# Kernel tuning notes

Hardware: AMD Instinct MI355X
Metric: run time of the kernel (lower is better)

## Reference

```python
import jax, jax.numpy as jnp
import numpy as np

EPS = 1e-5

def setup_inputs() -> dict:
    key = jax.random.key(0)
    k1, k2, k3 = jax.random.split(key, 3)
    x = jax.random.normal(k1, (16, 256, 32, 32), dtype=jnp.float32)
    embed = jax.random.normal(k2, (8192, 256), dtype=jnp.float32)
    cluster_size = jax.random.uniform(k3, (8192,), dtype=jnp.float32)
    return {"x": x, "embed": embed, "cluster_size": cluster_size}

def reference(x, embed, cluster_size):
    # x: (b, c, h, w) -> (b, h*w, c); project_in is Identity (codebook_dim == dim, heads=1)
    b, c, h, w = x.shape
    xt = jnp.transpose(x, (0, 2, 3, 1)).reshape(b, h * w, c)   # (b, n, d)
    flat = xt.reshape(-1, c)                                    # (N, d)
    d2 = (jnp.sum(flat * flat, axis=1, keepdims=True)
          - 2.0 * flat @ embed.T
          + jnp.sum(embed * embed, axis=1))                     # (N, K)
    embed_ind_flat = jnp.argmin(d2, axis=-1)                    # (N,) temperature==0 -> argmax of -d2
    quantize = embed[embed_ind_flat].reshape(b, h * w, c)       # gather codebook rows
    embed_ind = embed_ind_flat.reshape(b, h * w)
    # perplexity over (unnormalized) EMA cluster sizes, as in the torch code
    probs = cluster_size
    perplexity = jnp.exp(-jnp.sum(probs * jnp.log(probs + EPS)))
    # eval-mode commitment loss (weight_loss=True, commitment_weight=1.0)
    commit_loss = jnp.mean((quantize - xt) ** 2)
    return quantize, embed_ind, perplexity, commit_loss
```

## Files before the change

kernel.cpp:

```cpp
#include <hip/hip_runtime.h>
#include <hip/hip_bf16.h>
#include <math.h>

typedef _Float16 f16x8 __attribute__((ext_vector_type(8)));
typedef float f32x4 __attribute__((ext_vector_type(4)));

#define N_TOK 16384
#define D 256
#define K 8192

#define Q_OFF 0
#define IND_OFF 4194304
#define PERP_OFF 4210688
#define COMMIT_OFF 4210689

#define WS_CAND   0u
#define WS_E2     1048576u
#define WS_DSUM   1081344u
#define WS_EH     1114112u
#define WS_XH     5308416u
#define WS_XT     13697024u
#define WS_NEED   30474240u

__device__ __forceinline__ unsigned int ford(float f) {
    unsigned int u = __float_as_uint(f);
    return (u & 0x80000000u) ? ~u : (u | 0x80000000u);
}
__device__ __forceinline__ unsigned short f2h(float f) {
    _Float16 h = (_Float16)f;
    return *(unsigned short*)&h;
}
__device__ __forceinline__ void gload16(const void* g, void* l) {
    __builtin_amdgcn_global_load_lds(
        (const __attribute__((address_space(1))) unsigned int*)g,
        (__attribute__((address_space(3))) unsigned int*)l, 16, 0, 0);
}


__global__ void vq_convert_x(const float* __restrict__ x, float* __restrict__ xt,
                             unsigned short* __restrict__ xh) {
    __shared__ float t[64][65];
    const int tid = threadIdx.x;
    const int p0 = blockIdx.x * 64, c0 = blockIdx.y * 64, b = blockIdx.z;
    const int q = tid & 15, h = tid >> 4;
    #pragma unroll
    for (int r = 0; r < 4; ++r) {
        const int cl = r * 16 + h;
        const float4 v = *(const float4*)(x + (((size_t)(b * 256 + c0 + cl)) << 10) + p0 + q * 4);
        t[cl][q * 4 + 0] = v.x; t[cl][q * 4 + 1] = v.y;
        t[cl][q * 4 + 2] = v.z; t[cl][q * 4 + 3] = v.w;
    }
    __syncthreads();
    #pragma unroll
    for (int r = 0; r < 4; ++r) {
        const int nl = r * 16 + h;
        const int n = (b << 10) + p0 + nl;
        const int c = c0 + q * 4;
        float4 vf; ushort4 vh;
        vf.x = t[q * 4 + 0][nl]; vf.y = t[q * 4 + 1][nl];
        vf.z = t[q * 4 + 2][nl]; vf.w = t[q * 4 + 3][nl];
        vh.x = f2h(vf.x); vh.y = f2h(vf.y); vh.z = f2h(vf.z); vh.w = f2h(vf.w);
        *(float4*)(xt + ((size_t)n << 8) + c) = vf;
        *(ushort4*)(xh + ((size_t)n << 8) + c) = vh;
    }
}

__global__ void vq_prep_e(const float* __restrict__ e, unsigned short* __restrict__ eh,
                          float* __restrict__ e2, double* __restrict__ dsum) {
    if (blockIdx.x == 0 && threadIdx.x == 0) *dsum = 0.0;
    const int wave = threadIdx.x >> 6, lane = threadIdx.x & 63;
    const int c = blockIdx.x * 4 + wave;
    const float4 v = *(const float4*)(e + (size_t)c * D + lane * 4);
    ushort4 vh;
    vh.x = f2h(v.x); vh.y = f2h(v.y); vh.z = f2h(v.z); vh.w = f2h(v.w);
    *(ushort4*)(eh + (size_t)c * D + lane * 4) = vh;
    float s = v.x * v.x + v.y * v.y + v.z * v.z + v.w * v.w;
    #pragma unroll
    for (int off = 32; off > 0; off >>= 1) s += __shfl_down(s, off, 64);
    if (lane == 0) e2[c] = s;
}

__global__ __launch_bounds__(256)
__attribute__((amdgpu_waves_per_eu(2, 2)))
void vq_mfma_kernel(
    const unsigned short* __restrict__ xh, const unsigned short* __restrict__ eh,
    const float* __restrict__ e2, unsigned int* __restrict__ cand) {
    __shared__ __align__(16) unsigned short Bs[3][32 * 256];
    __shared__ float e2s[1024];

    const int tid = threadIdx.x;
    const int lane = tid & 63, wid = tid >> 6;
    const int l15 = lane & 15, lg = lane >> 4;
    const int split = blockIdx.y;
    const int m0 = blockIdx.x * 256;
    const int c0s = split * 1024;
    const int rw = m0 + wid * 64;

    *(float4*)&e2s[tid * 4] = *(const float4*)(e2 + c0s + tid * 4);

    f16x8 a[4][8];
    #pragma unroll
    for (int mf = 0; mf < 4; ++mf) {
        const unsigned short* ap = xh + (((size_t)(rw + mf * 16 + l15)) << 8) + lg * 8;
        #pragma unroll
        for (int t = 0; t < 8; ++t)
            a[mf][t] = *(const f16x8*)(ap + t * 32);
    }
    #pragma unroll
    for (int mf = 0; mf < 4; ++mf)
        #pragma unroll
        for (int t = 0; t < 8; ++t)
            asm volatile("" : "+v"(*(f32x4*)&a[mf][t]));

    __syncthreads();

    const int r0 = tid >> 5, cc = tid & 31;
    const unsigned short* ebase =
        eh + (((size_t)(c0s + r0)) << 8) + ((cc ^ (r0 & 7)) << 3);
    char* wdst = (char*)Bs + tid * 16;

    auto stage = [&](int t, int bo) {
        const unsigned short* p = ebase + t * 8192;
        #pragma unroll
        for (int i = 0; i < 4; ++i)
            gload16(p + i * 2048, wdst + bo + i * 4096);
    };

    const int rb0 = l15 * 512;
    const int rb1 = rb0 + 16 * 512;
    const int rx = l15 & 7;
    const char* wb = (const char*)Bs;

    float d1[16], d2[16];
    unsigned int ipk[16];
    #pragma unroll
    for (int r = 0; r < 16; ++r) { d1[r] = INFINITY; d2[r] = INFINITY; ipk[r] = 0; }

    int bo0 = 0, bo1 = 16384, bo2 = 32768;
    stage(0, bo0);
    stage(1, bo1);

    #pragma unroll 1
    for (int t = 0; t < 32; ++t) {
        if (t < 31) asm volatile("s_waitcnt vmcnt(4)" ::: "memory");
        else        asm volatile("s_waitcnt vmcnt(0)" ::: "memory");
        __builtin_amdgcn_s_barrier();
        if (t < 30) stage(t + 2, bo2);

        const float e2v0 = e2s[t * 32 + l15];
        const float e2v1 = e2s[t * 32 + 16 + l15];
        f32x4 acc[4][2];
        #pragma unroll
        for (int mf = 0; mf < 4; ++mf) {
            f32x4 z = {0.f, 0.f, 0.f, 0.f};
            acc[mf][0] = z; acc[mf][1] = z;
        }
        __builtin_amdgcn_s_setprio(1);
        #pragma unroll
        for (int ks = 0; ks < 4; ++ks) {
            #pragma unroll
            for (int ks2 = 0; ks2 < 2; ++ks2) {
                const int kc = ks * 8 + ks2 * 4;
                const int ko = ((kc + lg) ^ rx) << 4;
                const f16x8 b0 = *(const f16x8*)(wb + bo0 + rb0 + ko);
                const f16x8 b1 = *(const f16x8*)(wb + bo0 + rb1 + ko);
                #pragma unroll
                for (int mf = 0; mf < 4; ++mf) {
                    acc[mf][0] = __builtin_amdgcn_mfma_f32_16x16x32_f16(
                        a[mf][ks * 2 + ks2], b0, acc[mf][0], 0, 0, 0);
                    acc[mf][1] = __builtin_amdgcn_mfma_f32_16x16x32_f16(
                        a[mf][ks * 2 + ks2], b1, acc[mf][1], 0, 0, 0);
                }
            }
        }
        __builtin_amdgcn_s_setprio(0);

        const unsigned int cl0 = (unsigned int)(t * 32 + l15);
        #pragma unroll
        for (int mf = 0; mf < 4; ++mf) {
            #pragma unroll
            for (int reg = 0; reg < 4; ++reg) {
                const int rr = mf * 4 + reg;
                const float sc0 = fmaf(-2.0f, acc[mf][0][reg], e2v0);
                const float sc1 = fmaf(-2.0f, acc[mf][1][reg], e2v1);
                if (fminf(sc0, sc1) < d2[rr]) {
                    {
                        const bool lt1 = sc0 < d1[rr], lt2 = sc0 < d2[rr];
                        const unsigned int ii = ipk[rr];
                        const unsigned int nif = (ii << 16) | cl0;
                        const unsigned int nis = (ii & 0xFFFFu) | (cl0 << 16);
                        d2[rr] = lt1 ? d1[rr] : (lt2 ? sc0 : d2[rr]);
                        ipk[rr] = lt1 ? nif : (lt2 ? nis : ii);
                        d1[rr] = lt1 ? sc0 : d1[rr];
                    }
                    {
                        const unsigned int cl1 = cl0 + 16;
                        const bool lt1 = sc1 < d1[rr], lt2 = sc1 < d2[rr];
                        const unsigned int ii = ipk[rr];
                        const unsigned int nif = (ii << 16) | cl1;
                        const unsigned int nis = (ii & 0xFFFFu) | (cl1 << 16);
                        d2[rr] = lt1 ? d1[rr] : (lt2 ? sc1 : d2[rr]);
                        ipk[rr] = lt1 ? nif : (lt2 ? nis : ii);
                        d1[rr] = lt1 ? sc1 : d1[rr];
                    }
                }
            }
        }
        const int tmp = bo0; bo0 = bo1; bo1 = bo2; bo2 = tmp;
    }

    unsigned long long p1[16], p2[16];
    #pragma unroll
    for (int r = 0; r < 16; ++r) {
        p1[r] = (((unsigned long long)ford(d1[r])) << 32) |
                (unsigned int)(c0s + (ipk[r] & 0xFFFFu));
        p2[r] = (((unsigned long long)ford(d2[r])) << 32) |
                (unsigned int)(c0s + (ipk[r] >> 16));
    }
    #pragma unroll
    for (int st = 1; st < 16; st <<= 1) {
        #pragma unroll
        for (int r = 0; r < 16; ++r) {
            const unsigned long long q1 = __shfl_xor(p1[r], st, 64);
            const unsigned long long q2 = __shfl_xor(p2[r], st, 64);
            const unsigned long long n1 = p1[r] < q1 ? p1[r] : q1;
            const unsigned long long hi = p1[r] < q1 ? q1 : p1[r];
            const unsigned long long l2 = p2[r] < q2 ? p2[r] : q2;
            p1[r] = n1;
            p2[r] = hi < l2 ? hi : l2;
        }
    }
    if (l15 == 0) {
        #pragma unroll
        for (int mf = 0; mf < 4; ++mf)
            #pragma unroll
            for (int reg = 0; reg < 4; ++reg) {
                const int n = rw + mf * 16 + lg * 4 + reg;
                unsigned int* cp = cand + (((size_t)n) << 4) + split * 2;
                cp[0] = (unsigned int)p1[mf * 4 + reg];
                cp[1] = (unsigned int)p2[mf * 4 + reg];
            }
    }
}

__global__ void vq_rescore_finalize(const float* __restrict__ xt, const float* __restrict__ embed,
                                    const float* __restrict__ e2,
                                    const unsigned int* __restrict__ cand,
                                    float* __restrict__ out, double* __restrict__ dsum) {
    __shared__ double red[4];
    const int tid = threadIdx.x, wid = tid >> 6, lane = tid & 63;
    double wsum = 0.0;
    #pragma unroll 1
    for (int it = 0; it < 8; ++it) {
        const int n = blockIdx.x * 32 + it * 4 + wid;
        const float4 xv = *(const float4*)(xt + (((size_t)n) << 8) + lane * 4);
        unsigned long long best = 0xFFFFFFFFFFFFFFFFull;
        #pragma unroll 2
        for (int j = 0; j < 16; ++j) {
            const unsigned int c = cand[(((size_t)n) << 4) + j];
            const float4 ev = *(const float4*)(embed + (((size_t)c) << 8) + lane * 4);
            float dt = xv.x * ev.x + xv.y * ev.y + xv.z * ev.z + xv.w * ev.w;
            #pragma unroll
            for (int off = 32; off > 0; off >>= 1) dt += __shfl_xor(dt, off, 64);
            const float s = fmaf(-2.0f, dt, e2[c]);
            const unsigned long long p = (((unsigned long long)ford(s)) << 32) | c;
            best = p < best ? p : best;
        }
        const unsigned int bi = (unsigned int)(best & 0xFFFFFFFFull);
        if (lane == 0) out[IND_OFF + n] = (float)bi;
        const float4 ev = *(const float4*)(embed + (((size_t)bi) << 8) + lane * 4);
        *(float4*)(out + Q_OFF + (((size_t)n) << 8) + lane * 4) = ev;
        const float q0 = ev.x - xv.x, q1 = ev.y - xv.y, q2 = ev.z - xv.z, q3 = ev.w - xv.w;
        float a4 = q0 * q0 + q1 * q1 + q2 * q2 + q3 * q3;
        #pragma unroll
        for (int off = 32; off > 0; off >>= 1) a4 += __shfl_xor(a4, off, 64);
        if (lane == 0) wsum += (double)a4;
    }
    if (lane == 0) red[wid] = wsum;
    __syncthreads();
    if (tid == 0) atomicAdd(dsum, red[0] + red[1] + red[2] + red[3]);
}

__global__ void vq_tail_kernel(const float* __restrict__ cs,
                               const double* __restrict__ dsum,
                               float* __restrict__ out) {
    __shared__ double red[4];
    const int tid = threadIdx.x;
    double s = 0.0;
    for (int i = tid; i < K; i += 256) {
        const float p = cs[i];
        s += (double)(p * logf(p + 1e-5f));
    }
    #pragma unroll
    for (int off = 32; off > 0; off >>= 1) s += __shfl_down(s, off, 64);
    if ((tid & 63) == 0) red[tid >> 6] = s;
    __syncthreads();
    if (tid == 0) {
        const double tot = red[0] + red[1] + red[2] + red[3];
        const double pv = exp(-tot);
        out[PERP_OFF] = (pv > 3.3e38) ? 3.3e38f : (float)pv;
        out[COMMIT_OFF] = (float)(*dsum * (1.0 / 4194304.0));
    }
}

#define TM 64
#define TN 64
#define BKF 32
#define NSPLITF 2
#define CODES_PER_SPLIT (K / NSPLITF)
#define TILES_PER_SPLIT (CODES_PER_SPLIT / TN)

__global__ void vq_init_kernel(unsigned long long* __restrict__ keys, double* __restrict__ dsum) {
    int i = blockIdx.x * blockDim.x + threadIdx.x;
    if (i < N_TOK) keys[i] = 0xFFFFFFFFFFFFFFFFull;
    if (i == 0) *dsum = 0.0;
}
__global__ void vq_e2_kernel(const float* __restrict__ embed, float* __restrict__ e2) {
    int wave = threadIdx.x >> 6, lane = threadIdx.x & 63;
    int c = blockIdx.x * 4 + wave;
    const float4 v = *(const float4*)(embed + (size_t)c * D + lane * 4);
    float s = v.x * v.x + v.y * v.y + v.z * v.z + v.w * v.w;
    #pragma unroll
    for (int off = 32; off > 0; off >>= 1) s += __shfl_down(s, off, 64);
    if (lane == 0) e2[c] = s;
}
__global__ __launch_bounds__(256, 2) void vq_argmin_kernel(
    const float* __restrict__ x, const float* __restrict__ embed,
    const float* __restrict__ e2, unsigned long long* __restrict__ keys) {
    __shared__ float xT[D][TM];
    __shared__ float eT[BKF][TN + 4];
    const int tid = threadIdx.x;
    const int n0 = blockIdx.x * TM;
    const int b = n0 >> 10, p0 = n0 & 1023;
    const float* xb = x + (size_t)b * D * 1024 + p0;
    {
        const int t4 = (tid & 15) * 4, chb = tid >> 4;
        #pragma unroll
        for (int pass = 0; pass < 16; ++pass) {
            const int ch = pass * 16 + chb;
            *(float4*)&xT[ch][t4] = *(const float4*)(xb + (size_t)ch * 1024 + t4);
        }
    }
    __syncthreads();
    const int tm4 = (tid & 15) * 4, tn = tid >> 4, tn4 = tn * 4;
    float bestd[4]; int besti[4];
    #pragma unroll
    for (int i = 0; i < 4; ++i) { bestd[i] = INFINITY; besti[i] = 0x7fffffff; }
    for (int ct = 0; ct < TILES_PER_SPLIT; ++ct) {
        const int c0 = blockIdx.y * CODES_PER_SPLIT + ct * TN;
        float acc[4][4] = {};
        for (int kk = 0; kk < D; kk += BKF) {
            {
                const int j = tid >> 2, ch4 = (tid & 3) * 4;
                #pragma unroll
                for (int p = 0; p < 2; ++p) {
                    const int chl = p * 16 + ch4;
                    const float4 ev = *(const float4*)(embed + (size_t)(c0 + j) * D + kk + chl);
                    eT[chl + 0][j] = ev.x; eT[chl + 1][j] = ev.y;
                    eT[chl + 2][j] = ev.z; eT[chl + 3][j] = ev.w;
                }
            }
            __syncthreads();
            #pragma unroll
            for (int k2 = 0; k2 < BKF; ++k2) {
                const float4 a = *(const float4*)&xT[kk + k2][tm4];
                const float4 bv = *(const float4*)&eT[k2][tn4];
                acc[0][0] += a.x * bv.x; acc[0][1] += a.x * bv.y; acc[0][2] += a.x * bv.z; acc[0][3] += a.x * bv.w;
                acc[1][0] += a.y * bv.x; acc[1][1] += a.y * bv.y; acc[1][2] += a.y * bv.z; acc[1][3] += a.y * bv.w;
                acc[2][0] += a.z * bv.x; acc[2][1] += a.z * bv.y; acc[2][2] += a.z * bv.z; acc[2][3] += a.z * bv.w;
                acc[3][0] += a.w * bv.x; acc[3][1] += a.w * bv.y; acc[3][2] += a.w * bv.z; acc[3][3] += a.w * bv.w;
            }
            __syncthreads();
        }
        #pragma unroll
        for (int j = 0; j < 4; ++j) {
            const int c = c0 + tn4 + j;
            const float ec = e2[c];
            #pragma unroll
            for (int i = 0; i < 4; ++i) {
                const float s = ec - 2.0f * acc[i][j];
                if (s < bestd[i]) { bestd[i] = s; besti[i] = c; }
            }
        }
    }
    __syncthreads();
    float* cd = &eT[0][0];
    int* ci = (int*)&eT[16][0];
    #pragma unroll
    for (int i = 0; i < 4; ++i) { cd[tn * 64 + tm4 + i] = bestd[i]; ci[tn * 64 + tm4 + i] = besti[i]; }
    __syncthreads();
    if (tid < TM) {
        float bd = INFINITY; int bi = 0x7fffffff;
        for (int j = 0; j < 16; ++j) {
            const float d = cd[j * 64 + tid]; const int idx = ci[j * 64 + tid];
            if (d < bd || (d == bd && idx < bi)) { bd = d; bi = idx; }
        }
        atomicMin(&keys[n0 + tid], (((unsigned long long)ford(bd)) << 32) | (unsigned int)bi);
    }
}
__global__ void vq_finalize_kernel(const float* __restrict__ x, const float* __restrict__ embed,
                                   const unsigned long long* __restrict__ keys,
                                   float* __restrict__ out, double* __restrict__ dsum) {
    const int tid = threadIdx.x;
    const int n0 = blockIdx.x * 64;
    const int t = tid >> 2, q = tid & 3;
    const int n = n0 + t;
    const int b = n >> 10, p = n & 1023;
    if (tid < 64) {
        const int nn = n0 + tid;
        out[IND_OFF + nn] = (float)(int)(unsigned int)(keys[nn] & 0xFFFFFFFFull);
    }
    const int idx = (int)(unsigned int)(keys[n] & 0xFFFFFFFFull);
    const float* erow = embed + (size_t)idx * D;
    const float* xrow = x + (size_t)b * D * 1024 + p;
    float* qrow = out + Q_OFF + (size_t)n * D;
    float acc = 0.0f;
    #pragma unroll
    for (int i = 0; i < 16; ++i) {
        const int ch = i * 16 + q * 4;
        const float4 ev = *(const float4*)(erow + ch);
        *(float4*)(qrow + ch) = ev;
        const float x0 = xrow[(size_t)(ch + 0) * 1024];
        const float x1 = xrow[(size_t)(ch + 1) * 1024];
        const float x2 = xrow[(size_t)(ch + 2) * 1024];
        const float x3 = xrow[(size_t)(ch + 3) * 1024];
        const float d0 = ev.x - x0, d1 = ev.y - x1, d2 = ev.z - x2, d3 = ev.w - x3;
        acc += d0 * d0 + d1 * d1 + d2 * d2 + d3 * d3;
    }
    #pragma unroll
    for (int off = 32; off > 0; off >>= 1) acc += __shfl_down(acc, off, 64);
    if ((tid & 63) == 0) atomicAdd(dsum, (double)acc);
}

extern "C" void kernel_launch(void* const* d_in, const int* in_sizes, int n_in,
                              void* d_out, int out_size, void* d_ws, size_t ws_size,
                              hipStream_t stream) {
    const float* x = (const float*)d_in[0];
    const float* embed = (const float*)d_in[1];
    const float* cs = (const float*)d_in[2];
    float* out = (float*)d_out;
    char* ws = (char*)d_ws;

    if (ws_size >= (size_t)WS_NEED) {
        unsigned int* cand = (unsigned int*)(ws + WS_CAND);
        float* e2 = (float*)(ws + WS_E2);
        double* dsum = (double*)(ws + WS_DSUM);
        unsigned short* eh = (unsigned short*)(ws + WS_EH);
        unsigned short* xh = (unsigned short*)(ws + WS_XH);
        float* xt = (float*)(ws + WS_XT);

        vq_prep_e<<<dim3(K / 4), dim3(256), 0, stream>>>(embed, eh, e2, dsum);
        vq_convert_x<<<dim3(16, 4, 16), dim3(256), 0, stream>>>(x, xt, xh);
        vq_mfma_kernel<<<dim3(64, 8), dim3(256), 0, stream>>>(xh, eh, e2, cand);
        vq_rescore_finalize<<<dim3(512), dim3(256), 0, stream>>>(xt, embed, e2, cand, out, dsum);
        vq_tail_kernel<<<dim3(1), dim3(256), 0, stream>>>(cs, dsum, out);
    } else {
        unsigned long long* keys = (unsigned long long*)ws;
        float* e2 = (float*)(ws + 131072);
        double* dsum = (double*)(ws + 163840);
        vq_init_kernel<<<dim3(64), dim3(256), 0, stream>>>(keys, dsum);
        vq_e2_kernel<<<dim3(K / 4), dim3(256), 0, stream>>>(embed, e2);
        vq_argmin_kernel<<<dim3(N_TOK / TM, NSPLITF), dim3(256), 0, stream>>>(x, embed, e2, keys);
        vq_finalize_kernel<<<dim3(256), dim3(256), 0, stream>>>(x, embed, keys, out, dsum);
        vq_tail_kernel<<<dim3(1), dim3(256), 0, stream>>>(cs, dsum, out);
    }
}
```

Measured before the change: 173.2 us.

## Switch to double-buffered 64-row codebook tiles with software-prefetched LDS fragments

Replaces the triple-buffered 32-row codebook staging with two 64-row buffers, so each barrier covers twice as much work and there are half as many iterations. Within a tile, the B fragments for the next k-step are loaded from LDS before the current MFMAs issue, a register-level software pipeline. The change also drops the setprio hints and waits for all outstanding loads (vmcnt(0)) before every barrier. That wait removes the two-ahead prefetch depth, which risks exposing global load latency. The XOR swizzle now uses the full row index.

New measurement: 167.6 us. 3.3% less time.

```diff
diff --git a/kernel.cpp b/kernel.cpp
--- a/kernel.cpp
+++ b/kernel.cpp
@@ -85,7 +85,7 @@
 void vq_mfma_kernel(
     const unsigned short* __restrict__ xh, const unsigned short* __restrict__ eh,
     const float* __restrict__ e2, unsigned int* __restrict__ cand) {
-    __shared__ __align__(16) unsigned short Bs[3][32 * 256];
+    __shared__ __align__(16) unsigned short Bs[2][64 * 256];
     __shared__ float e2s[1024];
 
     const int tid = threadIdx.x;
@@ -116,97 +116,95 @@
 
     const int r0 = tid >> 5, cc = tid & 31;
     const unsigned short* ebase =
-        eh + (((size_t)(c0s + r0)) << 8) + ((cc ^ (r0 & 7)) << 3);
+        eh + (((size_t)(c0s + r0)) << 8) + ((cc ^ r0) << 3);
     char* wdst = (char*)Bs + tid * 16;
-
     auto stage = [&](int t, int bo) {
-        const unsigned short* p = ebase + t * 8192;
-        #pragma unroll
-        for (int i = 0; i < 4; ++i)
+        const unsigned short* p = ebase + t * 16384;
+        #pragma unroll
+        for (int i = 0; i < 8; ++i)
             gload16(p + i * 2048, wdst + bo + i * 4096);
     };
 
-    const int rb0 = l15 * 512;
-    const int rb1 = rb0 + 16 * 512;
-    const int rx = l15 & 7;
-    const char* wb = (const char*)Bs;
+    const char* rbase = (const char*)Bs + l15 * 512;
+    int ko[8];
+    #pragma unroll
+    for (int pr = 0; pr < 8; ++pr) ko[pr] = (((4 * pr + lg) ^ (l15 & 7)) << 4);
 
     float d1[16], d2[16];
     unsigned int ipk[16];
     #pragma unroll
     for (int r = 0; r < 16; ++r) { d1[r] = INFINITY; d2[r] = INFINITY; ipk[r] = 0; }
 
-    int bo0 = 0, bo1 = 16384, bo2 = 32768;
-    stage(0, bo0);
-    stage(1, bo1);
-
-    #pragma unroll 1
-    for (int t = 0; t < 32; ++t) {
-        if (t < 31) asm volatile("s_waitcnt vmcnt(4)" ::: "memory");
-        else        asm volatile("s_waitcnt vmcnt(0)" ::: "memory");
+    stage(0, 0);
+
+    #pragma unroll 2
+    for (int t = 0; t < 16; ++t) {
+        asm volatile("s_waitcnt vmcnt(0)" ::: "memory");
         __builtin_amdgcn_s_barrier();
-        if (t < 30) stage(t + 2, bo2);
-
-        const float e2v0 = e2s[t * 32 + l15];
-        const float e2v1 = e2s[t * 32 + 16 + l15];
-        f32x4 acc[4][2];
-        #pragma unroll
-        for (int mf = 0; mf < 4; ++mf) {
-            f32x4 z = {0.f, 0.f, 0.f, 0.f};
-            acc[mf][0] = z; acc[mf][1] = z;
-        }
-        __builtin_amdgcn_s_setprio(1);
-        #pragma unroll
-        for (int ks = 0; ks < 4; ++ks) {
-            #pragma unroll
-            for (int ks2 = 0; ks2 < 2; ++ks2) {
-                const int kc = ks * 8 + ks2 * 4;
-                const int ko = ((kc + lg) ^ rx) << 4;
-                const f16x8 b0 = *(const f16x8*)(wb + bo0 + rb0 + ko);
-                const f16x8 b1 = *(const f16x8*)(wb + bo0 + rb1 + ko);
+        if (t < 15) stage(t + 1, ((t + 1) & 1) * 32768);
+
+        const int BUF = (t & 1) * 32768;
+        #pragma unroll
+        for (int s2 = 0; s2 < 2; ++s2) {
+            const int sb = BUF + s2 * 16384;
+            const float e2v0 = e2s[t * 64 + s2 * 32 + l15];
+            const float e2v1 = e2s[t * 64 + s2 * 32 + 16 + l15];
+            f32x4 acc[4][2];
+            #pragma unroll
+            for (int mf = 0; mf < 4; ++mf) {
+                f32x4 z = {0.f, 0.f, 0.f, 0.f};
+                acc[mf][0] = z; acc[mf][1] = z;
+            }
+            f16x8 b0a = *(const f16x8*)(rbase + ko[0] + sb);
+            f16x8 b1a = *(const f16x8*)(rbase + ko[0] + sb + 8192);
+            #pragma unroll
+            for (int pr = 0; pr < 8; ++pr) {
+                f16x8 b0n, b1n;
+                if (pr < 7) {
+                    b0n = *(const f16x8*)(rbase + ko[pr + 1] + sb);
+                    b1n = *(const f16x8*)(rbase + ko[pr + 1] + sb + 8192);
+                }
                 #pragma unroll
                 for (int mf = 0; mf < 4; ++mf) {
                     acc[mf][0] = __builtin_amdgcn_mfma_f32_16x16x32_f16(
-                        a[mf][ks * 2 + ks2], b0, acc[mf][0], 0, 0, 0);
+                        a[mf][pr], b0a, acc[mf][0], 0, 0, 0);
                     acc[mf][1] = __builtin_amdgcn_mfma_f32_16x16x32_f16(
-                        a[mf][ks * 2 + ks2], b1, acc[mf][1], 0, 0, 0);
+                        a[mf][pr], b1a, acc[mf][1], 0, 0, 0);
                 }
-            }
-        }
-        __builtin_amdgcn_s_setprio(0);
-
-        const unsigned int cl0 = (unsigned int)(t * 32 + l15);
-        #pragma unroll
-        for (int mf = 0; mf < 4; ++mf) {
-            #pragma unroll
-            for (int reg = 0; reg < 4; ++reg) {
-                const int rr = mf * 4 + reg;
-                const float sc0 = fmaf(-2.0f, acc[mf][0][reg], e2v0);
-                const float sc1 = fmaf(-2.0f, acc[mf][1][reg], e2v1);
-                if (fminf(sc0, sc1) < d2[rr]) {
-                    {
-                        const bool lt1 = sc0 < d1[rr], lt2 = sc0 < d2[rr];
-                        const unsigned int ii = ipk[rr];
-                        const unsigned int nif = (ii << 16) | cl0;
-                        const unsigned int nis = (ii & 0xFFFFu) | (cl0 << 16);
-                        d2[rr] = lt1 ? d1[rr] : (lt2 ? sc0 : d2[rr]);
-                        ipk[rr] = lt1 ? nif : (lt2 ? nis : ii);
-                        d1[rr] = lt1 ? sc0 : d1[rr];
-                    }
-                    {
-                        const unsigned int cl1 = cl0 + 16;
-                        const bool lt1 = sc1 < d1[rr], lt2 = sc1 < d2[rr];
-                        const unsigned int ii = ipk[rr];
-                        const unsigned int nif = (ii << 16) | cl1;
-                        const unsigned int nis = (ii & 0xFFFFu) | (cl1 << 16);
-                        d2[rr] = lt1 ? d1[rr] : (lt2 ? sc1 : d2[rr]);
-                        ipk[rr] = lt1 ? nif : (lt2 ? nis : ii);
-                        d1[rr] = lt1 ? sc1 : d1[rr];
+                b0a = b0n; b1a = b1n;
+            }
+            const unsigned int cl0 = (unsigned int)(t * 64 + s2 * 32 + l15);
+            #pragma unroll
+            for (int mf = 0; mf < 4; ++mf) {
+                #pragma unroll
+                for (int reg = 0; reg < 4; ++reg) {
+                    const int rr = mf * 4 + reg;
+                    const float sc0 = fmaf(-2.0f, acc[mf][0][reg], e2v0);
+                    const float sc1 = fmaf(-2.0f, acc[mf][1][reg], e2v1);
+                    if (fminf(sc0, sc1) < d2[rr]) {
+                        {
+                            const bool lt1 = sc0 < d1[rr], lt2 = sc0 < d2[rr];
+                            const unsigned int ii = ipk[rr];
+                            const unsigned int nif = (ii << 16) | cl0;
+                            const unsigned int nis = (ii & 0xFFFFu) | (cl0 << 16);
+                            d2[rr] = lt1 ? d1[rr] : (lt2 ? sc0 : d2[rr]);
+                            ipk[rr] = lt1 ? nif : (lt2 ? nis : ii);
+                            d1[rr] = lt1 ? sc0 : d1[rr];
+                        }
+                        {
+                            const unsigned int cl1 = cl0 + 16;
+                            const bool lt1 = sc1 < d1[rr], lt2 = sc1 < d2[rr];
+                            const unsigned int ii = ipk[rr];
+                            const unsigned int nif = (ii << 16) | cl1;
+                            const unsigned int nis = (ii & 0xFFFFu) | (cl1 << 16);
+                            d2[rr] = lt1 ? d1[rr] : (lt2 ? sc1 : d2[rr]);
+                            ipk[rr] = lt1 ? nif : (lt2 ? nis : ii);
+                            d1[rr] = lt1 ? sc1 : d1[rr];
+                        }
                     }
                 }
             }
         }
-        const int tmp = bo0; bo0 = bo1; bo1 = bo2; bo2 = tmp;
     }
 
     unsigned long long p1[16], p2[16];
```

## Pre-swizzle codebook into MFMA fragment layout and load B directly from global

Applied to the files above, without the earlier changes.

The fp16 codebook is now written in a tiled layout that matches the MFMA B-operand fragment, so each lane can load its fragments with contiguous 16-byte global loads. The LDS triple-buffered async staging, barriers and waves-per-eu hint are removed, and the loop works on 16-column tiles instead of 32. This drops LDS traffic and per-tile block synchronisation, but B loads are no longer shared across the four waves (each wave fetches the same data, relying on L1/L2) and there is no explicit prefetch, so memory latency may be exposed.

Result: slower. 196.4 us (+13.4%).

```diff
diff --git a/kernel.cpp b/kernel.cpp
--- a/kernel.cpp
+++ b/kernel.cpp
@@ -29,11 +29,6 @@
 __device__ __forceinline__ unsigned short f2h(float f) {
     _Float16 h = (_Float16)f;
     return *(unsigned short*)&h;
-}
-__device__ __forceinline__ void gload16(const void* g, void* l) {
-    __builtin_amdgcn_global_load_lds(
-        (const __attribute__((address_space(1))) unsigned int*)g,
-        (__attribute__((address_space(3))) unsigned int*)l, 16, 0, 0);
 }
 
 
@@ -65,7 +60,7 @@
     }
 }
 
-__global__ void vq_prep_e(const float* __restrict__ e, unsigned short* __restrict__ eh,
+__global__ void vq_prep_e(const float* __restrict__ e, unsigned short* __restrict__ ehT,
                           float* __restrict__ e2, double* __restrict__ dsum) {
     if (blockIdx.x == 0 && threadIdx.x == 0) *dsum = 0.0;
     const int wave = threadIdx.x >> 6, lane = threadIdx.x & 63;
@@ -73,7 +68,9 @@
     const float4 v = *(const float4*)(e + (size_t)c * D + lane * 4);
     ushort4 vh;
     vh.x = f2h(v.x); vh.y = f2h(v.y); vh.z = f2h(v.z); vh.w = f2h(v.w);
-    *(ushort4*)(eh + (size_t)c * D + lane * 4) = vh;
+    unsigned short* dst = ehT + (((size_t)(c >> 4)) << 12) + ((lane >> 1) << 7) +
+                          ((c & 15) << 3) + ((lane & 1) << 2);
+    *(ushort4*)dst = vh;
     float s = v.x * v.x + v.y * v.y + v.z * v.z + v.w * v.w;
     #pragma unroll
     for (int off = 32; off > 0; off >>= 1) s += __shfl_down(s, off, 64);
@@ -81,11 +78,9 @@
 }
 
 __global__ __launch_bounds__(256)
-__attribute__((amdgpu_waves_per_eu(2, 2)))
 void vq_mfma_kernel(
-    const unsigned short* __restrict__ xh, const unsigned short* __restrict__ eh,
+    const unsigned short* __restrict__ xh, const unsigned short* __restrict__ ehT,
     const float* __restrict__ e2, unsigned int* __restrict__ cand) {
-    __shared__ __align__(16) unsigned short Bs[3][32 * 256];
     __shared__ float e2s[1024];
 
     const int tid = threadIdx.x;
@@ -106,107 +101,49 @@
         for (int t = 0; t < 8; ++t)
             a[mf][t] = *(const f16x8*)(ap + t * 32);
     }
-    #pragma unroll
-    for (int mf = 0; mf < 4; ++mf)
-        #pragma unroll
-        for (int t = 0; t < 8; ++t)
-            asm volatile("" : "+v"(*(f32x4*)&a[mf][t]));
-
-    __syncthreads();
-
-    const int r0 = tid >> 5, cc = tid & 31;
-    const unsigned short* ebase =
-        eh + (((size_t)(c0s + r0)) << 8) + ((cc ^ (r0 & 7)) << 3);
-    char* wdst = (char*)Bs + tid * 16;
-
-    auto stage = [&](int t, int bo) {
-        const unsigned short* p = ebase + t * 8192;
-        #pragma unroll
-        for (int i = 0; i < 4; ++i)
-            gload16(p + i * 2048, wdst + bo + i * 4096);
-    };
-
-    const int rb0 = l15 * 512;
-    const int rb1 = rb0 + 16 * 512;
-    const int rx = l15 & 7;
-    const char* wb = (const char*)Bs;
+    __syncthreads();
+
+    const char* bb = (const char*)ehT + (((size_t)c0s) << 9) + lane * 16;
 
     float d1[16], d2[16];
     unsigned int ipk[16];
     #pragma unroll
     for (int r = 0; r < 16; ++r) { d1[r] = INFINITY; d2[r] = INFINITY; ipk[r] = 0; }
 
-    int bo0 = 0, bo1 = 16384, bo2 = 32768;
-    stage(0, bo0);
-    stage(1, bo1);
-
     #pragma unroll 1
-    for (int t = 0; t < 32; ++t) {
-        if (t < 31) asm volatile("s_waitcnt vmcnt(4)" ::: "memory");
-        else        asm volatile("s_waitcnt vmcnt(0)" ::: "memory");
-        __builtin_amdgcn_s_barrier();
-        if (t < 30) stage(t + 2, bo2);
-
-        const float e2v0 = e2s[t * 32 + l15];
-        const float e2v1 = e2s[t * 32 + 16 + l15];
-        f32x4 acc[4][2];
+    for (int tile = 0; tile < 64; ++tile) {
+        const char* tb = bb + tile * 8192;
+        f16x8 b[8];
+        #pragma unroll
+        for (int j = 0; j < 8; ++j) b[j] = *(const f16x8*)(tb + j * 1024);
+        const float e2v = e2s[tile * 16 + l15];
+        f32x4 acc[4];
         #pragma unroll
         for (int mf = 0; mf < 4; ++mf) {
             f32x4 z = {0.f, 0.f, 0.f, 0.f};
-            acc[mf][0] = z; acc[mf][1] = z;
-        }
-        __builtin_amdgcn_s_setprio(1);
-        #pragma unroll
-        for (int ks = 0; ks < 4; ++ks) {
-            #pragma unroll
-            for (int ks2 = 0; ks2 < 2; ++ks2) {
-                const int kc = ks * 8 + ks2 * 4;
-                const int ko = ((kc + lg) ^ rx) << 4;
-                const f16x8 b0 = *(const f16x8*)(wb + bo0 + rb0 + ko);
-                const f16x8 b1 = *(const f16x8*)(wb + bo0 + rb1 + ko);
-                #pragma unroll
-                for (int mf = 0; mf < 4; ++mf) {
-                    acc[mf][0] = __builtin_amdgcn_mfma_f32_16x16x32_f16(
-                        a[mf][ks * 2 + ks2], b0, acc[mf][0], 0, 0, 0);
-                    acc[mf][1] = __builtin_amdgcn_mfma_f32_16x16x32_f16(
-                        a[mf][ks * 2 + ks2], b1, acc[mf][1], 0, 0, 0);
+            acc[mf] = z;
+        }
+        #pragma unroll
+        for (int j = 0; j < 8; ++j)
+            #pragma unroll
+            for (int mf = 0; mf < 4; ++mf)
+                acc[mf] = __builtin_amdgcn_mfma_f32_16x16x32_f16(
+                    a[mf][j], b[j], acc[mf], 0, 0, 0);
+        const unsigned int cl = (unsigned int)(tile * 16 + l15);
+        #pragma unroll
+        for (int mf = 0; mf < 4; ++mf)
+            #pragma unroll
+            for (int reg = 0; reg < 4; ++reg) {
+                const int rr = mf * 4 + reg;
+                const float s = fmaf(-2.0f, acc[mf][reg], e2v);
+                if (s < d2[rr]) {
+                    const bool lt1 = s < d1[rr];
+                    const unsigned int ii = ipk[rr];
+                    d2[rr] = lt1 ? d1[rr] : s;
+                    ipk[rr] = lt1 ? ((ii << 16) | cl) : ((ii & 0xFFFFu) | (cl << 16));
+                    d1[rr] = lt1 ? s : d1[rr];
                 }
             }
-        }
-        __builtin_amdgcn_s_setprio(0);
-
-        const unsigned int cl0 = (unsigned int)(t * 32 + l15);
-        #pragma unroll
-        for (int mf = 0; mf < 4; ++mf) {
-            #pragma unroll
-            for (int reg = 0; reg < 4; ++reg) {
-                const int rr = mf * 4 + reg;
-                const float sc0 = fmaf(-2.0f, acc[mf][0][reg], e2v0);
-                const float sc1 = fmaf(-2.0f, acc[mf][1][reg], e2v1);
-                if (fminf(sc0, sc1) < d2[rr]) {
-                    {
-                        const bool lt1 = sc0 < d1[rr], lt2 = sc0 < d2[rr];
-                        const unsigned int ii = ipk[rr];
-                        const unsigned int nif = (ii << 16) | cl0;
-                        const unsigned int nis = (ii & 0xFFFFu) | (cl0 << 16);
-                        d2[rr] = lt1 ? d1[rr] : (lt2 ? sc0 : d2[rr]);
-                        ipk[rr] = lt1 ? nif : (lt2 ? nis : ii);
-                        d1[rr] = lt1 ? sc0 : d1[rr];
-                    }
-                    {
-                        const unsigned int cl1 = cl0 + 16;
-                        const bool lt1 = sc1 < d1[rr], lt2 = sc1 < d2[rr];
-                        const unsigned int ii = ipk[rr];
-                        const unsigned int nif = (ii << 16) | cl1;
-                        const unsigned int nis = (ii & 0xFFFFu) | (cl1 << 16);
-                        d2[rr] = lt1 ? d1[rr] : (lt2 ? sc1 : d2[rr]);
-                        ipk[rr] = lt1 ? nif : (lt2 ? nis : ii);
-                        d1[rr] = lt1 ? sc1 : d1[rr];
-                    }
-                }
-            }
-        }
-        const int tmp = bo0; bo0 = bo1; bo1 = bo2; bo2 = tmp;
     }
 
     unsigned long long p1[16], p2[16];
@@ -445,13 +382,13 @@
         unsigned int* cand = (unsigned int*)(ws + WS_CAND);
         float* e2 = (float*)(ws + WS_E2);
         double* dsum = (double*)(ws + WS_DSUM);
-        unsigned short* eh = (unsigned short*)(ws + WS_EH);
+        unsigned short* ehT = (unsigned short*)(ws + WS_EH);
         unsigned short* xh = (unsigned short*)(ws + WS_XH);
         float* xt = (float*)(ws + WS_XT);
 
-        vq_prep_e<<<dim3(K / 4), dim3(256), 0, stream>>>(embed, eh, e2, dsum);
+        vq_prep_e<<<dim3(K / 4), dim3(256), 0, stream>>>(embed, ehT, e2, dsum);
         vq_convert_x<<<dim3(16, 4, 16), dim3(256), 0, stream>>>(x, xt, xh);
-        vq_mfma_kernel<<<dim3(64, 8), dim3(256), 0, stream>>>(xh, eh, e2, cand);
+        vq_mfma_kernel<<<dim3(64, 8), dim3(256), 0, stream>>>(xh, ehT, e2, cand);
         vq_rescore_finalize<<<dim3(512), dim3(256), 0, stream>>>(xt, embed, e2, cand, out, dsum);
         vq_tail_kernel<<<dim3(1), dim3(256), 0, stream>>>(cs, dsum, out);
     } else {
```
